# Kernel tuning notes

Measured on AMD Instinct MI355X. Metric: run time of the kernel, lower is better.

## Reference

```python
import jax, jax.numpy as jnp
import numpy as np

B, L, DIN = 16, 1024, 512
H, DH = 4, 128          # num_heads = 4, head_dim = in_features // 4
DEG = 16                # avg random in-degree (plus one self-loop per node)
NEG_SLOPE = 0.2         # DGL GATConv default leaky_relu slope


def setup_inputs() -> dict:
    key = jax.random.key(0)
    ks = jax.random.split(key, 8)
    N = B * L
    E = N * DEG
    src = jax.random.randint(ks[0], (E,), 0, N)
    dst = jax.random.randint(ks[1], (E,), 0, N)
    loops = jnp.arange(N)
    src = jnp.concatenate([src, loops])  # self-loops guarantee every dst has in-edges
    dst = jnp.concatenate([dst, loops])
    s = 1.0 / np.sqrt(DIN)
    text = jax.random.normal(ks[2], (B, L, DIN), jnp.float32)
    weight = jax.random.normal(ks[3], (DIN, DIN), jnp.float32) * s      # module's self.weight
    fc_w = jax.random.normal(ks[4], (DIN, H * DH), jnp.float32) * s     # GATConv fc (no bias)
    attn_l = jax.random.normal(ks[5], (H, DH), jnp.float32) * s
    attn_r = jax.random.normal(ks[6], (H, DH), jnp.float32) * s
    bias = jax.random.normal(ks[7], (DIN,), jnp.float32) * 0.01         # module's self.bias
    return {"text": text, "weight": weight, "fc_w": fc_w,
            "attn_l": attn_l, "attn_r": attn_r, "bias": bias,
            "src": src, "dst": dst}


def reference(text, weight, fc_w, attn_l, attn_r, bias, src, dst):
    b, l, d = text.shape
    N = b * l
    # outer linear projection
    hidden = jnp.einsum('bld,de->ble', text, weight)
    feat = hidden.reshape(N, d)
    # GATConv: fc projection to heads
    h = (feat @ fc_w).reshape(N, H, DH)                 # [N, H, DH]
    el = jnp.einsum('nhd,hd->nh', h, attn_l)            # [N, H]
    er = jnp.einsum('nhd,hd->nh', h, attn_r)            # [N, H]
    # edge attention logits (src contributes el, dst contributes er)
    e = jax.nn.leaky_relu(el[src] + er[dst], NEG_SLOPE)  # [E, H]
    # segment (per-destination) softmax, numerically stable
    emax = jax.ops.segment_max(e, dst, num_segments=N)   # [N, H]
    ex = jnp.exp(e - emax[dst])
    denom = jax.ops.segment_sum(ex, dst, num_segments=N)
    alpha = ex / denom[dst]                              # [E, H]
    # weighted message aggregation (scatter-add)
    m = h[src] * alpha[:, :, None]                       # [E, H, DH]
    out = jax.ops.segment_sum(m, dst, num_segments=N)    # [N, H, DH]
    return out.reshape(b, l, H * DH) + bias
```

## Files before the change

### kernel.cpp

```cpp
#include <hip/hip_runtime.h>
#include <stdint.h>

#define AS1 __attribute__((address_space(1)))
#define AS3 __attribute__((address_space(3)))

typedef __attribute__((ext_vector_type(8))) short short8;
typedef __attribute__((ext_vector_type(4))) float f32x4;

#define CAP 64
#define NGEMM 512
#define NSCAT 128
#define NW2T 256
#define NCVT 2048

__device__ __forceinline__ short f2bf(float f) {
  union { float f; unsigned u; } v; v.f = f;
  unsigned r = v.u + 0x7fffu + ((v.u >> 16) & 1u);
  return (short)(r >> 16);
}
__device__ __forceinline__ float bf_lo(unsigned w) { union { unsigned u; float f; } v; v.u = w << 16;          return v.f; }
__device__ __forceinline__ float bf_hi(unsigned w) { union { unsigned u; float f; } v; v.u = w & 0xffff0000u;  return v.f; }

__global__ __launch_bounds__(256) void k_w2t_cvt(const float* __restrict__ W,
                                                 const float* __restrict__ F,
                                                 const float* __restrict__ text,
                                                 short* __restrict__ W2t,
                                                 short* __restrict__ textb,
                                                 int* __restrict__ cnt) {
  const int tid = threadIdx.x;
  const int b   = blockIdx.x;

  if (b >= NW2T) {
    const size_t base = (size_t)(b - NW2T) * 4096 + tid * 16;
    const float4* p = (const float4*)(text + base);
    float4 a0 = p[0], a1 = p[1], a2 = p[2], a3 = p[3];
    short8 o0, o1;
    o0[0] = f2bf(a0.x); o0[1] = f2bf(a0.y); o0[2] = f2bf(a0.z); o0[3] = f2bf(a0.w);
    o0[4] = f2bf(a1.x); o0[5] = f2bf(a1.y); o0[6] = f2bf(a1.z); o0[7] = f2bf(a1.w);
    o1[0] = f2bf(a2.x); o1[1] = f2bf(a2.y); o1[2] = f2bf(a2.z); o1[3] = f2bf(a2.w);
    o1[4] = f2bf(a3.x); o1[5] = f2bf(a3.y); o1[6] = f2bf(a3.z); o1[7] = f2bf(a3.w);
    *(short8*)(textb + base) = o0;
    *(short8*)(textb + base + 8) = o1;
    return;
  }

  if (tid < 64) cnt[b * 64 + tid] = 0;

  __shared__ float sW[64][36];
  __shared__ float sF[64][36];
  const int bx = b & 15, by = b >> 4;
  const int d0 = bx * 32, j0 = by * 32;
  const int dx = tid & 15, jy = tid >> 4;
  float a00 = 0.f, a01 = 0.f, a10 = 0.f, a11 = 0.f;
  const int wr = tid >> 3, wc = (tid & 7) * 8;
  const int fr = tid >> 2, fc = (tid & 3) * 8;
  for (int e0 = 0; e0 < 512; e0 += 64) {
    float4 w0 = *(const float4*)&W[(size_t)(d0 + wr) * 512 + e0 + wc];
    float4 w1 = *(const float4*)&W[(size_t)(d0 + wr) * 512 + e0 + wc + 4];
    float4 f0 = *(const float4*)&F[(size_t)(e0 + fr) * 512 + j0 + fc];
    float4 f1 = *(const float4*)&F[(size_t)(e0 + fr) * 512 + j0 + fc + 4];
    sW[wc + 0][wr] = w0.x; sW[wc + 1][wr] = w0.y; sW[wc + 2][wr] = w0.z; sW[wc + 3][wr] = w0.w;
    sW[wc + 4][wr] = w1.x; sW[wc + 5][wr] = w1.y; sW[wc + 6][wr] = w1.z; sW[wc + 7][wr] = w1.w;
    *(float4*)&sF[fr][fc] = f0;
    *(float4*)&sF[fr][fc + 4] = f1;
    __syncthreads();
#pragma unroll
    for (int e = 0; e < 64; ++e) {
      float2 w2 = *(const float2*)&sW[e][dx * 2];
      float2 f2 = *(const float2*)&sF[e][jy * 2];
      a00 += w2.x * f2.x; a01 += w2.x * f2.y;
      a10 += w2.y * f2.x; a11 += w2.y * f2.y;
    }
    __syncthreads();
  }
  short* o0 = W2t + (size_t)(j0 + jy * 2) * 512 + d0 + dx * 2;
  o0[0] = f2bf(a00); o0[1] = f2bf(a10);
  o0[512] = f2bf(a01); o0[513] = f2bf(a11);
}

__global__ __launch_bounds__(256) void k_gemm_scatter(const short* __restrict__ A,
                                                      const short* __restrict__ Bt,
                                                      short* __restrict__ Cs,
                                                      float* __restrict__ el,
                                                      float* __restrict__ er,
                                                      const float* __restrict__ attn_l,
                                                      const float* __restrict__ attn_r,
                                                      const int* __restrict__ src,
                                                      const int* __restrict__ dst,
                                                      int* __restrict__ cnt,
                                                      int* __restrict__ bucket,
                                                      int E, int N) {
  const int tid = threadIdx.x;
  if (blockIdx.x >= NGEMM) {
    for (int e = (blockIdx.x - NGEMM) * 256 + tid; e < E; e += NSCAT * 256) {
      int d = dst[e];
      int p = atomicAdd(&cnt[d], 1);
      if (p < CAP) bucket[(size_t)d * CAP + p] = src[e];
    }
    return;
  }

  __shared__ __align__(16) short sA[2][128 * 64];
  __shared__ __align__(16) short sB[2][128 * 64];
  __shared__ float sEl[128][2];
  __shared__ float sEr[128][2];
  const int bx   = blockIdx.x;
  const int xcd  = bx & 7, kk = bx >> 3;
  const int bm0  = (xcd * 16 + (kk & 15)) * 128;
  const int hh   = kk >> 4;
  const int bn0  = hh * 128;
  const int lane = tid & 63;
  const int wid  = tid >> 6;
  const int wm   = wid >> 1;
  const int wn   = wid & 1;
  const int cc   = lane & 15;

  f32x4 acc[4][4] = {};

  const int srow  = tid >> 3;
  const int sslot = (tid & 7) ^ (srow & 7);
  const int lslot = tid & 7;

#pragma unroll
  for (int r = 0; r < 4; ++r) {
    int row = r * 32 + srow;
    __builtin_amdgcn_global_load_lds((const AS1 void*)(A + (size_t)(bm0 + row) * 512 + sslot * 8),
                                     (AS3 void*)(sA[0] + row * 64 + lslot * 8), 16, 0, 0);
    __builtin_amdgcn_global_load_lds((const AS1 void*)(Bt + (size_t)(bn0 + row) * 512 + sslot * 8),
                                     (AS3 void*)(sB[0] + row * 64 + lslot * 8), 16, 0, 0);
  }
  __syncthreads();

  for (int kt = 0; kt < 8; ++kt) {
    const int cur = kt & 1;
    if (kt < 7) {
      const int kbase = (kt + 1) * 64;
#pragma unroll
      for (int r = 0; r < 4; ++r) {
        int row = r * 32 + srow;
        __builtin_amdgcn_global_load_lds((const AS1 void*)(A + (size_t)(bm0 + row) * 512 + kbase + sslot * 8),
                                         (AS3 void*)(sA[cur ^ 1] + row * 64 + lslot * 8), 16, 0, 0);
        __builtin_amdgcn_global_load_lds((const AS1 void*)(Bt + (size_t)(bn0 + row) * 512 + kbase + sslot * 8),
                                         (AS3 void*)(sB[cur ^ 1] + row * 64 + lslot * 8), 16, 0, 0);
      }
    }
#pragma unroll
    for (int ks = 0; ks < 2; ++ks) {
      short8 af[4], bfr[4];
#pragma unroll
      for (int i = 0; i < 4; ++i) {
        int row  = wm * 64 + i * 16 + cc;
        int slot = (ks * 4 + (lane >> 4)) ^ (row & 7);
        af[i] = *(const short8*)(sA[cur] + row * 64 + slot * 8);
      }
#pragma unroll
      for (int j = 0; j < 4; ++j) {
        int row  = wn * 64 + j * 16 + cc;
        int slot = (ks * 4 + (lane >> 4)) ^ (row & 7);
        bfr[j] = *(const short8*)(sB[cur] + row * 64 + slot * 8);
      }
#pragma unroll
      for (int i = 0; i < 4; ++i)
#pragma unroll
        for (int j = 0; j < 4; ++j)
          acc[i][j] = __builtin_amdgcn_mfma_f32_16x16x32_bf16(af[i], bfr[j], acc[i][j], 0, 0, 0);
    }
    __syncthreads();
  }

  const int r4 = (lane >> 4) * 4;
#pragma unroll
  for (int i = 0; i < 4; ++i)
#pragma unroll
    for (int j = 0; j < 4; ++j) {
      int cin = wn * 64 + j * 16 + cc;
#pragma unroll
      for (int rg = 0; rg < 4; ++rg) {
        int gr = bm0 + wm * 64 + i * 16 + r4 + rg;
        Cs[((size_t)hh * N + gr) * 128 + cin] = f2bf(acc[i][j][rg]);
      }
    }
  float alv[4], arv[4];
#pragma unroll
  for (int j = 0; j < 4; ++j) {
    int cl = wn * 64 + j * 16 + cc;
    alv[j] = attn_l[hh * 128 + cl];
    arv[j] = attn_r[hh * 128 + cl];
  }
#pragma unroll
  for (int i = 0; i < 4; ++i)
#pragma unroll
    for (int rg = 0; rg < 4; ++rg) {
      float pl = 0.f, pr = 0.f;
#pragma unroll
      for (int j = 0; j < 4; ++j) {
        float v = acc[i][j][rg];
        pl += v * alv[j]; pr += v * arv[j];
      }
#pragma unroll
      for (int d = 1; d < 16; d <<= 1) {
        pl += __shfl_xor(pl, d);
        pr += __shfl_xor(pr, d);
      }
      if (cc == 0) {
        int row = wm * 64 + i * 16 + r4 + rg;
        sEl[row][wn] = pl;
        sEr[row][wn] = pr;
      }
    }
  __syncthreads();
  if (tid < 128) {
    int gr = bm0 + tid;
    el[gr * 4 + hh] = sEl[tid][0] + sEl[tid][1];
    er[gr * 4 + hh] = sEr[tid][0] + sEr[tid][1];
  }
}

__global__ __launch_bounds__(256) void k_aggregate(const int* __restrict__ cnt, const int* __restrict__ bucket,
                                                   const float* __restrict__ el, const float* __restrict__ er,
                                                   const short* __restrict__ hs, const float* __restrict__ bias,
                                                   float* __restrict__ out, int N) {
  const int b    = blockIdx.x;
  const int s    = (b >> 1) & 3;
  const int nt   = (b >> 3) * 2 + (b & 1);
  const int nd0  = nt * 8 + (threadIdx.x >> 6);
  const int nd1  = nd0 + 4;
  const int lane = threadIdx.x & 63;
  const int g    = lane >> 4;
  const int cl   = lane & 15;

  int n0_raw = cnt[nd0];
  int n1_raw = cnt[nd1];
  int i0_raw = bucket[(size_t)nd0 * CAP + lane];
  int i1_raw = bucket[(size_t)nd1 * CAP + lane];
  float ern0 = er[nd0 * 4 + s];
  float ern1 = er[nd1 * 4 + s];

  int n0 = (n0_raw < CAP) ? n0_raw : CAP;
  int n1 = (n1_raw < CAP) ? n1_raw : CAP;
  int idx0 = (lane < n0) ? i0_raw : 0;
  int idx1 = (lane < n1) ? i1_raw : 0;
  float x0 = el[idx0 * 4 + s] + ern0;
  float x1 = el[idx1 * 4 + s] + ern1;
  x0 = (x0 > 0.f) ? x0 : 0.2f * x0;
  x1 = (x1 > 0.f) ? x1 : 0.2f * x1;
  float wgt0 = (lane < n0) ? __expf(x0) : 0.f;
  float wgt1 = (lane < n1) ? __expf(x1) : 0.f;

  const short* hbase = hs + (size_t)s * N * 128;
  float acc0[8], acc1[8];
#pragma unroll
  for (int j = 0; j < 8; ++j) { acc0[j] = 0.f; acc1[j] = 0.f; }
  float sw0 = 0.f, sw1 = 0.f;

  const int maxn = (n0 > n1) ? n0 : n1;
  for (int base = 0; base < maxn; base += 8) {
    if (base < n0) {
      int e0 = base + g, e1 = base + 4 + g;
      int s0 = __shfl(idx0, e0), s1 = __shfl(idx0, e1);
      float w0 = __shfl(wgt0, e0), w1 = __shfl(wgt0, e1);
      uint4 v0 = ((const uint4*)(hbase + (size_t)s0 * 128))[cl];
      uint4 v1 = ((const uint4*)(hbase + (size_t)s1 * 128))[cl];
      sw0 += w0 + w1;
      acc0[0] += w0 * bf_lo(v0.x) + w1 * bf_lo(v1.x);
      acc0[1] += w0 * bf_hi(v0.x) + w1 * bf_hi(v1.x);
      acc0[2] += w0 * bf_lo(v0.y) + w1 * bf_lo(v1.y);
      acc0[3] += w0 * bf_hi(v0.y) + w1 * bf_hi(v1.y);
      acc0[4] += w0 * bf_lo(v0.z) + w1 * bf_lo(v1.z);
      acc0[5] += w0 * bf_hi(v0.z) + w1 * bf_hi(v1.z);
      acc0[6] += w0 * bf_lo(v0.w) + w1 * bf_lo(v1.w);
      acc0[7] += w0 * bf_hi(v0.w) + w1 * bf_hi(v1.w);
    }
    if (base < n1) {
      int e0 = base + g, e1 = base + 4 + g;
      int s0 = __shfl(idx1, e0), s1 = __shfl(idx1, e1);
      float w0 = __shfl(wgt1, e0), w1 = __shfl(wgt1, e1);
      uint4 v0 = ((const uint4*)(hbase + (size_t)s0 * 128))[cl];
      uint4 v1 = ((const uint4*)(hbase + (size_t)s1 * 128))[cl];
      sw1 += w0 + w1;
      acc1[0] += w0 * bf_lo(v0.x) + w1 * bf_lo(v1.x);
      acc1[1] += w0 * bf_hi(v0.x) + w1 * bf_hi(v1.x);
      acc1[2] += w0 * bf_lo(v0.y) + w1 * bf_lo(v1.y);
      acc1[3] += w0 * bf_hi(v0.y) + w1 * bf_hi(v1.y);
      acc1[4] += w0 * bf_lo(v0.z) + w1 * bf_lo(v1.z);
      acc1[5] += w0 * bf_hi(v0.z) + w1 * bf_hi(v1.z);
      acc1[6] += w0 * bf_lo(v0.w) + w1 * bf_lo(v1.w);
      acc1[7] += w0 * bf_hi(v0.w) + w1 * bf_hi(v1.w);
    }
  }

#pragma unroll
  for (int d = 16; d < 64; d <<= 1) {
    sw0 += __shfl_xor(sw0, d);
    sw1 += __shfl_xor(sw1, d);
#pragma unroll
    for (int j = 0; j < 8; ++j) {
      acc0[j] += __shfl_xor(acc0[j], d);
      acc1[j] += __shfl_xor(acc1[j], d);
    }
  }

  if (g == 0) {
    int c0 = s * 128 + cl * 8;
    float4 b0 = *(const float4*)(bias + c0);
    float4 b1 = *(const float4*)(bias + c0 + 4);
    {
      float inv = 1.f / sw0;
      float4 o0, o1;
      o0.x = acc0[0] * inv + b0.x; o0.y = acc0[1] * inv + b0.y;
      o0.z = acc0[2] * inv + b0.z; o0.w = acc0[3] * inv + b0.w;
      o1.x = acc0[4] * inv + b1.x; o1.y = acc0[5] * inv + b1.y;
      o1.z = acc0[6] * inv + b1.z; o1.w = acc0[7] * inv + b1.w;
      float* op = out + (size_t)nd0 * 512 + c0;
      *(float4*)op = o0;
      *(float4*)(op + 4) = o1;
    }
    {
      float inv = 1.f / sw1;
      float4 o0, o1;
      o0.x = acc1[0] * inv + b0.x; o0.y = acc1[1] * inv + b0.y;
      o0.z = acc1[2] * inv + b0.z; o0.w = acc1[3] * inv + b0.w;
      o1.x = acc1[4] * inv + b1.x; o1.y = acc1[5] * inv + b1.y;
      o1.z = acc1[6] * inv + b1.z; o1.w = acc1[7] * inv + b1.w;
      float* op = out + (size_t)nd1 * 512 + c0;
      *(float4*)op = o0;
      *(float4*)(op + 4) = o1;
    }
  }
}

extern "C" void kernel_launch(void* const* d_in, const int* in_sizes, int n_in,
                              void* d_out, int out_size, void* d_ws, size_t ws_size,
                              hipStream_t stream) {
  const float* text   = (const float*)d_in[0];
  const float* weight = (const float*)d_in[1];
  const float* fcw    = (const float*)d_in[2];
  const float* attn_l = (const float*)d_in[3];
  const float* attn_r = (const float*)d_in[4];
  const float* bias   = (const float*)d_in[5];
  const int*   src    = (const int*)d_in[6];
  const int*   dst    = (const int*)d_in[7];
  const int E = in_sizes[6];
  const int N = in_sizes[0] / 512;

  char* ws = (char*)d_ws;
  size_t o = 0;
  auto carve = [&](size_t bytes) { void* p = ws + o; o = (o + bytes + 255) & ~(size_t)255; return p; };
  short* w2t    = (short*)carve((size_t)512 * 512 * 2);
  short* textb  = (short*)carve((size_t)N * 512 * 2);
  short* hs     = (short*)carve((size_t)N * 512 * 2);
  float* el     = (float*)carve((size_t)N * 4 * 4);
  float* er     = (float*)carve((size_t)N * 4 * 4);
  int*   cnt    = (int*)carve((size_t)N * 4);
  int*   bucket = (int*)carve((size_t)N * CAP * 4);

  k_w2t_cvt<<<NW2T + NCVT, 256, 0, stream>>>(weight, fcw, text, w2t, textb, cnt);
  k_gemm_scatter<<<NGEMM + NSCAT, 256, 0, stream>>>(textb, w2t, hs, el, er, attn_l, attn_r,
                                                    src, dst, cnt, bucket, E, N);
  k_aggregate<<<N * 4 / 8, 256, 0, stream>>>(cnt, bucket, el, er, hs, bias, (float*)d_out, N);
}
```

Before: 81.95 us.

## Double text-convert work per block, unroll GEMM k-loop, pack gather accumulators

The text-to-bf16 conversion now has each thread handle 32 floats, which halves the number of conversion blocks. The GEMM main k-loop gets a full unroll pragma. The gather/aggregation accumulators become float2 vectors so the compiler can emit packed FMA instructions. Together these aim to cut launch/block overhead and ALU instruction count, at the cost of more registers per thread and some risk from the pointer-cast aliasing of the vector accumulators.

```diff
diff --git a/kernel.cpp b/kernel.cpp
--- a/kernel.cpp
+++ b/kernel.cpp
@@ -6,12 +6,13 @@
 
 typedef __attribute__((ext_vector_type(8))) short short8;
 typedef __attribute__((ext_vector_type(4))) float f32x4;
+typedef __attribute__((ext_vector_type(2))) float f32x2;
 
 #define CAP 64
 #define NGEMM 512
 #define NSCAT 128
 #define NW2T 256
-#define NCVT 2048
+#define NCVT 1024
 
 __device__ __forceinline__ short f2bf(float f) {
   union { float f; unsigned u; } v; v.f = f;
@@ -20,6 +21,7 @@
 }
 __device__ __forceinline__ float bf_lo(unsigned w) { union { unsigned u; float f; } v; v.u = w << 16;          return v.f; }
 __device__ __forceinline__ float bf_hi(unsigned w) { union { unsigned u; float f; } v; v.u = w & 0xffff0000u;  return v.f; }
+__device__ __forceinline__ f32x2 bf2x(unsigned w) { f32x2 r; r.x = bf_lo(w); r.y = bf_hi(w); return r; }
 
 __global__ __launch_bounds__(256) void k_w2t_cvt(const float* __restrict__ W,
                                                  const float* __restrict__ F,
@@ -31,16 +33,20 @@
   const int b   = blockIdx.x;
 
   if (b >= NW2T) {
-    const size_t base = (size_t)(b - NW2T) * 4096 + tid * 16;
+    const size_t base = (size_t)(b - NW2T) * 8192 + tid * 32;
     const float4* p = (const float4*)(text + base);
-    float4 a0 = p[0], a1 = p[1], a2 = p[2], a3 = p[3];
-    short8 o0, o1;
-    o0[0] = f2bf(a0.x); o0[1] = f2bf(a0.y); o0[2] = f2bf(a0.z); o0[3] = f2bf(a0.w);
-    o0[4] = f2bf(a1.x); o0[5] = f2bf(a1.y); o0[6] = f2bf(a1.z); o0[7] = f2bf(a1.w);
-    o1[0] = f2bf(a2.x); o1[1] = f2bf(a2.y); o1[2] = f2bf(a2.z); o1[3] = f2bf(a2.w);
-    o1[4] = f2bf(a3.x); o1[5] = f2bf(a3.y); o1[6] = f2bf(a3.z); o1[7] = f2bf(a3.w);
-    *(short8*)(textb + base) = o0;
-    *(short8*)(textb + base + 8) = o1;
+    float4 a[8];
+#pragma unroll
+    for (int s = 0; s < 8; ++s) a[s] = p[s];
+#pragma unroll
+    for (int s = 0; s < 4; ++s) {
+      short8 o;
+      o[0] = f2bf(a[2 * s].x); o[1] = f2bf(a[2 * s].y);
+      o[2] = f2bf(a[2 * s].z); o[3] = f2bf(a[2 * s].w);
+      o[4] = f2bf(a[2 * s + 1].x); o[5] = f2bf(a[2 * s + 1].y);
+      o[6] = f2bf(a[2 * s + 1].z); o[7] = f2bf(a[2 * s + 1].w);
+      *(short8*)(textb + base + s * 8) = o;
+    }
     return;
   }
 
@@ -131,6 +137,7 @@
   }
   __syncthreads();
 
+#pragma unroll
   for (int kt = 0; kt < 8; ++kt) {
     const int cur = kt & 1;
     if (kt < 7) {
@@ -248,9 +255,9 @@
   float wgt1 = (lane < n1) ? __expf(x1) : 0.f;
 
   const short* hbase = hs + (size_t)s * N * 128;
-  float acc0[8], acc1[8];
-#pragma unroll
-  for (int j = 0; j < 8; ++j) { acc0[j] = 0.f; acc1[j] = 0.f; }
+  f32x2 acc0[4], acc1[4];
+#pragma unroll
+  for (int j = 0; j < 4; ++j) { acc0[j] = (f32x2)0.f; acc1[j] = (f32x2)0.f; }
   float sw0 = 0.f, sw1 = 0.f;
 
   const int maxn = (n0 > n1) ? n0 : n1;
@@ -262,14 +269,10 @@
       uint4 v0 = ((const uint4*)(hbase + (size_t)s0 * 128))[cl];
       uint4 v1 = ((const uint4*)(hbase + (size_t)s1 * 128))[cl];
       sw0 += w0 + w1;
-      acc0[0] += w0 * bf_lo(v0.x) + w1 * bf_lo(v1.x);
-      acc0[1] += w0 * bf_hi(v0.x) + w1 * bf_hi(v1.x);
-      acc0[2] += w0 * bf_lo(v0.y) + w1 * bf_lo(v1.y);
-      acc0[3] += w0 * bf_hi(v0.y) + w1 * bf_hi(v1.y);
-      acc0[4] += w0 * bf_lo(v0.z) + w1 * bf_lo(v1.z);
-      acc0[5] += w0 * bf_hi(v0.z) + w1 * bf_hi(v1.z);
-      acc0[6] += w0 * bf_lo(v0.w) + w1 * bf_lo(v1.w);
-      acc0[7] += w0 * bf_hi(v0.w) + w1 * bf_hi(v1.w);
+      acc0[0] += w0 * bf2x(v0.x) + w1 * bf2x(v1.x);
+      acc0[1] += w0 * bf2x(v0.y) + w1 * bf2x(v1.y);
+      acc0[2] += w0 * bf2x(v0.z) + w1 * bf2x(v1.z);
+      acc0[3] += w0 * bf2x(v0.w) + w1 * bf2x(v1.w);
     }
     if (base < n1) {
       int e0 = base + g, e1 = base + 4 + g;
@@ -278,25 +281,23 @@
       uint4 v0 = ((const uint4*)(hbase + (size_t)s0 * 128))[cl];
       uint4 v1 = ((const uint4*)(hbase + (size_t)s1 * 128))[cl];
       sw1 += w0 + w1;
-      acc1[0] += w0 * bf_lo(v0.x) + w1 * bf_lo(v1.x);
-      acc1[1] += w0 * bf_hi(v0.x) + w1 * bf_hi(v1.x);
-      acc1[2] += w0 * bf_lo(v0.y) + w1 * bf_lo(v1.y);
-      acc1[3] += w0 * bf_hi(v0.y) + w1 * bf_hi(v1.y);
-      acc1[4] += w0 * bf_lo(v0.z) + w1 * bf_lo(v1.z);
-      acc1[5] += w0 * bf_hi(v0.z) + w1 * bf_hi(v1.z);
-      acc1[6] += w0 * bf_lo(v0.w) + w1 * bf_lo(v1.w);
-      acc1[7] += w0 * bf_hi(v0.w) + w1 * bf_hi(v1.w);
-    }
-  }
-
+      acc1[0] += w0 * bf2x(v0.x) + w1 * bf2x(v1.x);
+      acc1[1] += w0 * bf2x(v0.y) + w1 * bf2x(v1.y);
+      acc1[2] += w0 * bf2x(v0.z) + w1 * bf2x(v1.z);
+      acc1[3] += w0 * bf2x(v0.w) + w1 * bf2x(v1.w);
+    }
+  }
+
+  float* a0 = (float*)acc0;
+  float* a1 = (float*)acc1;
 #pragma unroll
   for (int d = 16; d < 64; d <<= 1) {
     sw0 += __shfl_xor(sw0, d);
     sw1 += __shfl_xor(sw1, d);
 #pragma unroll
     for (int j = 0; j < 8; ++j) {
-      acc0[j] += __shfl_xor(acc0[j], d);
-      acc1[j] += __shfl_xor(acc1[j], d);
+      a0[j] += __shfl_xor(a0[j], d);
+      a1[j] += __shfl_xor(a1[j], d);
     }
   }
 
@@ -307,10 +308,10 @@
     {
       float inv = 1.f / sw0;
       float4 o0, o1;
-      o0.x = acc0[0] * inv + b0.x; o0.y = acc0[1] * inv + b0.y;
-      o0.z = acc0[2] * inv + b0.z; o0.w = acc0[3] * inv + b0.w;
-      o1.x = acc0[4] * inv + b1.x; o1.y = acc0[5] * inv + b1.y;
-      o1.z = acc0[6] * inv + b1.z; o1.w = acc0[7] * inv + b1.w;
+      o0.x = a0[0] * inv + b0.x; o0.y = a0[1] * inv + b0.y;
+      o0.z = a0[2] * inv + b0.z; o0.w = a0[3] * inv + b0.w;
+      o1.x = a0[4] * inv + b1.x; o1.y = a0[5] * inv + b1.y;
+      o1.z = a0[6] * inv + b1.z; o1.w = a0[7] * inv + b1.w;
       float* op = out + (size_t)nd0 * 512 + c0;
       *(float4*)op = o0;
       *(float4*)(op + 4) = o1;
@@ -318,10 +319,10 @@
     {
       float inv = 1.f / sw1;
       float4 o0, o1;
-      o0.x = acc1[0] * inv + b0.x; o0.y = acc1[1] * inv + b0.y;
-      o0.z = acc1[2] * inv + b0.z; o0.w = acc1[3] * inv + b0.w;
-      o1.x = acc1[4] * inv + b1.x; o1.y = acc1[5] * inv + b1.y;
-      o1.z = acc1[6] * inv + b1.z; o1.w = acc1[7] * inv + b1.w;
+      o0.x = a1[0] * inv + b0.x; o0.y = a1[1] * inv + b0.y;
+      o0.z = a1[2] * inv + b0.z; o0.w = a1[3] * inv + b0.w;
+      o1.x = a1[4] * inv + b1.x; o1.y = a1[5] * inv + b1.y;
+      o1.z = a1[6] * inv + b1.z; o1.w = a1[7] * inv + b1.w;
       float* op = out + (size_t)nd1 * 512 + c0;
       *(float4*)op = o0;
       *(float4*)(op + 4) = o1;
```

Result: no change. 82.51 us (+0.7%).
